# Performance work log

Measured on AMD Instinct MI355X. Metric: run time of the kernel, lower is better.

## Reference

```python
import jax, jax.numpy as jnp
import numpy as np

N = 50000      # nodes
E = 1_600_000  # edges
D = 512        # input_dim == embedding_dim (see notes: fc_emb output is dead code)
H = 256        # hidden_channels
G = 16         # graphs in the batch


def setup_inputs() -> dict:
    key = jax.random.key(0)
    ks = jax.random.split(key, 16)
    x = jax.random.normal(ks[0], (N, D), dtype=jnp.float32)
    edge_index = jax.random.randint(ks[1], (2, E), 0, N, dtype=jnp.int64)
    batch = jnp.sort(jax.random.randint(ks[2], (N,), 0, G, dtype=jnp.int64))

    def lin(k, fi, fo):
        s = 1.0 / np.sqrt(fi)
        return jax.random.uniform(k, (fi, fo), jnp.float32, -s, s)

    return {
        "x": x,
        "edge_index": edge_index,
        "batch": batch,
        "W1": lin(ks[3], D, H), "b1": jnp.zeros((H,), jnp.float32),
        "W2": lin(ks[4], H, H), "b2": jnp.zeros((H,), jnp.float32),
        "W3": lin(ks[5], H, H), "b3": jnp.zeros((H,), jnp.float32),
        "Wf": lin(ks[6], H, 64), "bf": jnp.zeros((64,), jnp.float32),
        "Wp": lin(ks[7], 64, 1), "bp": jnp.zeros((1,), jnp.float32),
    }


def _gcn_conv(h, src, dst, norm, W, b):
    # GCNConv: out[i] = sum_{j->i} norm_ji * (h[j] @ W) + b  (self-loops included in src/dst)
    m = h @ W                                    # [N, out]  transform first (smaller gather)
    agg = jax.ops.segment_sum(m[src] * norm[:, None], dst, num_segments=N)
    return agg + b


def reference(x, edge_index, batch, W1, b1, W2, b2, W3, b3, Wf, bf, Wp, bp):
    loops = jnp.arange(N, dtype=edge_index.dtype)
    src = jnp.concatenate([edge_index[0], loops])   # [E+N]
    dst = jnp.concatenate([edge_index[1], loops])
    # symmetric normalization D^{-1/2} (A+I) D^{-1/2}; degree over targets incl. self-loops
    deg = jax.ops.segment_sum(jnp.ones_like(dst, jnp.float32), dst, num_segments=N)
    dinv = jnp.where(deg > 0, jax.lax.rsqrt(deg), 0.0)
    norm = dinv[src] * dinv[dst]                    # [E+N]

    h = jax.nn.relu(_gcn_conv(x, src, dst, norm, W1, b1))
    h = jax.nn.relu(_gcn_conv(h, src, dst, norm, W2, b2))
    h = _gcn_conv(h, src, dst, norm, W3, b3)

    # global_mean_pool over graph ids
    counts = jax.ops.segment_sum(jnp.ones((N,), jnp.float32), batch, num_segments=G)
    pooled = jax.ops.segment_sum(h, batch, num_segments=G) / jnp.maximum(counts, 1.0)[:, None]

    # dropout treated as identity (eval-mode determinism for baseline)
    out = pooled @ Wf + bf
    out = out @ Wp + bp
    return jax.nn.sigmoid(out)
```

## Files before the change

kernel.cpp:

```cpp
#include <hip/hip_runtime.h>
#include <hip/hip_bf16.h>

#define NN 50000
#define EE 1600000
#define DD 512
#define HH 256
#define GG 16
#define BK 96
#define NCH 256
#define CHSZ 6250

typedef long fp8x8;
typedef __attribute__((ext_vector_type(4))) float f32x4;
typedef __attribute__((ext_vector_type(2))) float f32x2;

__device__ __forceinline__ float b2f(unsigned short s) {
    union { unsigned int i; float f; } v; v.i = ((unsigned int)s) << 16; return v.f;
}
__device__ __forceinline__ unsigned char f2fp8(float f) {
    return (unsigned char)(__builtin_amdgcn_cvt_pk_fp8_f32(f, f, 0, false) & 0xff);
}
__device__ __forceinline__ unsigned int pk4fp8(float a, float b, float c, float d) {
    unsigned int r = __builtin_amdgcn_cvt_pk_fp8_f32(a, b, 0, false);
    return __builtin_amdgcn_cvt_pk_fp8_f32(c, d, r, true);
}

__global__ __launch_bounds__(256) void k_hist_cvt(const int* __restrict__ ei,
                                                  unsigned int* __restrict__ histg,
                                                  const float* __restrict__ x, unsigned char* __restrict__ xb,
                                                  const float* __restrict__ W1, const float* __restrict__ W2,
                                                  const float* __restrict__ W3, unsigned char* __restrict__ W1t,
                                                  unsigned char* __restrict__ W2t, unsigned char* __restrict__ W3t) {
    __shared__ unsigned int hp[6250];
    int b = blockIdx.x, t = threadIdx.x;
    if (b < 1024) {
        int j = b >> 2, q = b & 3;
        int dlo = q * 12500;
        for (int i = t; i < 6250; i += 256) hp[i] = 0;
        __syncthreads();
        int base = j * CHSZ;
        for (int k = 0; k < 25; ++k) {
            int o = k * 256 + t;
            if (o < CHSZ) {
                int d = ei[EE + base + o];
                unsigned int ld = (unsigned)(d - dlo);
                if (ld < 12500u) atomicAdd(&hp[ld >> 1], (ld & 1) ? 65536u : 1u);
            }
        }
        __syncthreads();
        unsigned int* dst = histg + j * 25000 + q * 6250;
        for (int i = t; i < 6250; i += 256) dst[i] = hp[i];
    } else if (b < 7274) {
        size_t i0 = ((size_t)(b - 1024) * 256 + t) * 16;
        float4 v0 = *(const float4*)(x + i0);
        float4 v1 = *(const float4*)(x + i0 + 4);
        float4 v2 = *(const float4*)(x + i0 + 8);
        float4 v3 = *(const float4*)(x + i0 + 12);
        uint4 o;
        o.x = pk4fp8(v0.x, v0.y, v0.z, v0.w);
        o.y = pk4fp8(v1.x, v1.y, v1.z, v1.w);
        o.z = pk4fp8(v2.x, v2.y, v2.z, v2.w);
        o.w = pk4fp8(v3.x, v3.y, v3.z, v3.w);
        *(uint4*)(xb + i0) = o;
    } else {
        int u = (b - 7274) * 256 + t;
        if (u < 131072) {
            int k = u >> 8, n = u & 255;
            W1t[(size_t)n * 512 + k] = f2fp8(W1[u]);
        } else if (u < 196608) {
            int q = u - 131072; int k = q >> 8, n = q & 255;
            W2t[(size_t)n * 256 + k] = f2fp8(W2[q]);
        } else {
            int q = u - 196608; int k = q >> 8, n = q & 255;
            W3t[(size_t)n * 256 + k] = f2fp8(W3[q]);
        }
    }
}

__global__ __launch_bounds__(256) void k_scan(const unsigned int* __restrict__ histg,
                                              unsigned int* __restrict__ offg,
                                              int* __restrict__ cnt, float* __restrict__ dinv) {
    __shared__ unsigned int part[8][32];
    int t = threadIdx.x;
    int il = t & 31, g = t >> 5;
    int i = blockIdx.x * 32 + il;
    bool ok = (i < 25000);
    unsigned int hv[32];
    unsigned int p0 = 0, p1 = 0;
    if (ok) {
        const unsigned int* hp = histg + (size_t)(g * 32) * 25000 + i;
        #pragma unroll
        for (int jj = 0; jj < 32; ++jj) hv[jj] = hp[(size_t)jj * 25000];
        #pragma unroll
        for (int jj = 0; jj < 32; ++jj) { p0 += hv[jj] & 0xffffu; p1 += hv[jj] >> 16; }
    }
    part[g][il] = p0 | (p1 << 16);
    __syncthreads();
    unsigned int b0 = 0, b1 = 0;
    #pragma unroll
    for (int g2 = 0; g2 < 7; ++g2) {
        if (g2 < g) { unsigned int p = part[g2][il]; b0 += p & 0xffffu; b1 += p >> 16; }
    }
    if (ok && g == 7) {
        unsigned int tot0 = b0 + p0, tot1 = b1 + p1;
        cnt[2 * i]     = (int)tot0;
        cnt[2 * i + 1] = (int)tot1;
        dinv[2 * i]     = rsqrtf((float)tot0 + 1.0f);
        dinv[2 * i + 1] = rsqrtf((float)tot1 + 1.0f);
    }
    if (ok) {
        unsigned int run0 = b0, run1 = b1;
        unsigned int* op = offg + (size_t)(g * 32) * 25000 + i;
        #pragma unroll
        for (int jj = 0; jj < 32; ++jj) {
            op[(size_t)jj * 25000] = run0 | (run1 << 16);
            run0 += hv[jj] & 0xffffu; run1 += hv[jj] >> 16;
        }
    }
}

__global__ __launch_bounds__(256) void k_place(const int* __restrict__ ei,
                                               const unsigned int* __restrict__ offg,
                                               unsigned short* __restrict__ bucket) {
    __shared__ unsigned int cur[3125];
    int b = blockIdx.x, t = threadIdx.x;
    int x8 = b & 7, j = b >> 3;
    int lo = x8 * CHSZ;
    for (int i = t; i < 3125; i += 256) cur[i] = 0;
    __syncthreads();
    int base = j * CHSZ;
    for (int k = 0; k < 25; ++k) {
        int o = k * 256 + t;
        if (o < CHSZ) {
            int d = ei[EE + base + o];
            unsigned ld = (unsigned)(d - lo);
            if (ld < 6250u) {
                int s = ei[base + o];
                unsigned old = atomicAdd(&cur[ld >> 1], (ld & 1) ? 65536u : 1u);
                unsigned rank = (ld & 1) ? (old >> 16) : (old & 0xffffu);
                unsigned ov = offg[j * 25000 + (d >> 1)];
                unsigned pos = ((d & 1) ? (ov >> 16) : (ov & 0xffffu)) + rank;
                if (pos < BK) bucket[(size_t)d * BK + pos] = (unsigned short)s;
            }
        }
    }
}

__global__ __launch_bounds__(256) void k_gemm_fp8(const unsigned char* __restrict__ A,
                                                  const unsigned char* __restrict__ Bt,
                                                  const float* __restrict__ dinv,
                                                  unsigned char* __restrict__ C, int M, int K) {
    __shared__ unsigned char As[128 * 32];
    __shared__ unsigned char Bs[128 * 32];
    const int tid  = threadIdx.x;
    const int wave = tid >> 6;
    const int lane = tid & 63;
    const int row0 = blockIdx.x * 128;
    const int col0 = blockIdx.y * 128;
    const int wr = wave & 1;
    const int wc = wave >> 1;
    const int l15 = lane & 15;
    const int quad = lane >> 4;

    const int sr = tid >> 1;
    const int sk = (tid & 1) * 16;

    int ar = row0 + sr; if (ar >= M) ar = M - 1;
    const int bc = col0 + sr;

    f32x4 acc[4][4];
    #pragma unroll
    for (int i = 0; i < 4; ++i)
        #pragma unroll
        for (int j = 0; j < 4; ++j)
            acc[i][j] = (f32x4){0.f, 0.f, 0.f, 0.f};

    for (int kb = 0; kb < K; kb += 32) {
        const unsigned char* ga = A + (size_t)ar * K + kb + sk;
        const unsigned char* gb = Bt + (size_t)bc * K + kb + sk;
        __builtin_amdgcn_global_load_lds((const __attribute__((address_space(1))) void*)ga,
            (__attribute__((address_space(3))) void*)&As[wave * 1024], 16, 0, 0);
        __builtin_amdgcn_global_load_lds((const __attribute__((address_space(1))) void*)gb,
            (__attribute__((address_space(3))) void*)&Bs[wave * 1024], 16, 0, 0);
        __syncthreads();

        fp8x8 af[4], bfr[4];
        #pragma unroll
        for (int mi = 0; mi < 4; ++mi)
            af[mi] = *(const fp8x8*)&As[(wr * 64 + mi * 16 + l15) * 32 + quad * 8];
        #pragma unroll
        for (int ni = 0; ni < 4; ++ni)
            bfr[ni] = *(const fp8x8*)&Bs[(wc * 64 + ni * 16 + l15) * 32 + quad * 8];
        #pragma unroll
        for (int mi = 0; mi < 4; ++mi)
            #pragma unroll
            for (int ni = 0; ni < 4; ++ni)
                acc[mi][ni] = __builtin_amdgcn_mfma_f32_16x16x32_fp8_fp8(af[mi], bfr[ni], acc[mi][ni], 0, 0, 0);
        __syncthreads();
    }

    #pragma unroll
    for (int mi = 0; mi < 4; ++mi) {
        #pragma unroll
        for (int r = 0; r < 4; ++r) {
            int grow = row0 + wr * 64 + mi * 16 + quad * 4 + r;
            if (grow < M) {
                float ds = dinv[grow];
                #pragma unroll
                for (int ni = 0; ni < 4; ++ni) {
                    int gcol = col0 + wc * 64 + ni * 16 + l15;
                    C[(size_t)grow * 256 + gcol] = f2fp8(ds * acc[mi][ni][r]);
                }
            }
        }
    }
}

__global__ __launch_bounds__(256) void k_agg(const unsigned int* __restrict__ m,
                                             const float* __restrict__ bias,
                                             const float* __restrict__ dinv, const int* __restrict__ cnt,
                                             const unsigned short* __restrict__ bucket,
                                             unsigned int* __restrict__ outb,
                                             int do_relu) {
    int lane = threadIdx.x & 63;
    int node = blockIdx.x * 4 + (threadIdx.x >> 6);
    if (node >= NN) return;
    const unsigned int* mrow = m + lane;
    unsigned int v = mrow[(size_t)node * 64];
    f32x2 lo = __builtin_amdgcn_cvt_pk_f32_fp8(v, false);
    f32x2 hi = __builtin_amdgcn_cvt_pk_f32_fp8(v, true);
    float4 acc = make_float4(lo.x, lo.y, hi.x, hi.y);
    int n = cnt[node]; if (n > BK) n = BK;
    const unsigned short* cs = bucket + (size_t)node * BK;
    int p = 0;
    for (; p + 8 <= n; p += 8) {
        int s0 = cs[p], s1 = cs[p + 1], s2 = cs[p + 2], s3 = cs[p + 3];
        int s4 = cs[p + 4], s5 = cs[p + 5], s6 = cs[p + 6], s7 = cs[p + 7];
        unsigned int u0 = mrow[(size_t)s0 * 64];
        unsigned int u1 = mrow[(size_t)s1 * 64];
        unsigned int u2 = mrow[(size_t)s2 * 64];
        unsigned int u3 = mrow[(size_t)s3 * 64];
        unsigned int u4 = mrow[(size_t)s4 * 64];
        unsigned int u5 = mrow[(size_t)s5 * 64];
        unsigned int u6 = mrow[(size_t)s6 * 64];
        unsigned int u7 = mrow[(size_t)s7 * 64];
        f32x2 a0 = __builtin_amdgcn_cvt_pk_f32_fp8(u0, false), b0 = __builtin_amdgcn_cvt_pk_f32_fp8(u0, true);
        f32x2 a1 = __builtin_amdgcn_cvt_pk_f32_fp8(u1, false), b1 = __builtin_amdgcn_cvt_pk_f32_fp8(u1, true);
        f32x2 a2 = __builtin_amdgcn_cvt_pk_f32_fp8(u2, false), b2 = __builtin_amdgcn_cvt_pk_f32_fp8(u2, true);
        f32x2 a3 = __builtin_amdgcn_cvt_pk_f32_fp8(u3, false), b3 = __builtin_amdgcn_cvt_pk_f32_fp8(u3, true);
        f32x2 a4 = __builtin_amdgcn_cvt_pk_f32_fp8(u4, false), b4 = __builtin_amdgcn_cvt_pk_f32_fp8(u4, true);
        f32x2 a5 = __builtin_amdgcn_cvt_pk_f32_fp8(u5, false), b5 = __builtin_amdgcn_cvt_pk_f32_fp8(u5, true);
        f32x2 a6 = __builtin_amdgcn_cvt_pk_f32_fp8(u6, false), b6 = __builtin_amdgcn_cvt_pk_f32_fp8(u6, true);
        f32x2 a7 = __builtin_amdgcn_cvt_pk_f32_fp8(u7, false), b7 = __builtin_amdgcn_cvt_pk_f32_fp8(u7, true);
        acc.x += ((a0.x + a1.x) + (a2.x + a3.x)) + ((a4.x + a5.x) + (a6.x + a7.x));
        acc.y += ((a0.y + a1.y) + (a2.y + a3.y)) + ((a4.y + a5.y) + (a6.y + a7.y));
        acc.z += ((b0.x + b1.x) + (b2.x + b3.x)) + ((b4.x + b5.x) + (b6.x + b7.x));
        acc.w += ((b0.y + b1.y) + (b2.y + b3.y)) + ((b4.y + b5.y) + (b6.y + b7.y));
    }
    for (; p < n; ++p) {
        int s = cs[p];
        unsigned int u = mrow[(size_t)s * 64];
        f32x2 a = __builtin_amdgcn_cvt_pk_f32_fp8(u, false);
        f32x2 b = __builtin_amdgcn_cvt_pk_f32_fp8(u, true);
        acc.x += a.x; acc.y += a.y; acc.z += b.x; acc.w += b.y;
    }
    float di = dinv[node];
    const float4 bb = *(const float4*)(bias + lane * 4);
    acc.x = acc.x * di + bb.x; acc.y = acc.y * di + bb.y;
    acc.z = acc.z * di + bb.z; acc.w = acc.w * di + bb.w;
    if (do_relu) {
        acc.x = fmaxf(acc.x, 0.f); acc.y = fmaxf(acc.y, 0.f);
        acc.z = fmaxf(acc.z, 0.f); acc.w = fmaxf(acc.w, 0.f);
    }
    outb[(size_t)node * 64 + lane] = pk4fp8(acc.x, acc.y, acc.z, acc.w);
}

__global__ __launch_bounds__(256) void k_pool(const unsigned int* __restrict__ h,
                                              const int* __restrict__ batch,
                                              float* __restrict__ pooled, float* __restrict__ cnts) {
    __shared__ float pl[GG * 256];
    __shared__ float cl[GG];
    int t = threadIdx.x;
    for (int i = t; i < GG * 256; i += 256) pl[i] = 0.f;
    if (t < GG) cl[t] = 0.f;
    __syncthreads();
    int sub = t >> 6;
    int fd = t & 63;
    int chunk = (NN + gridDim.x - 1) / gridDim.x;
    int i0 = blockIdx.x * chunk;
    int i1 = i0 + chunk; if (i1 > NN) i1 = NN;
    int gcur = -1;
    float a0 = 0.f, a1 = 0.f, a2 = 0.f, a3 = 0.f, cr = 0.f;
    for (int i = i0 + sub; i < i1; i += 4) {
        int g = batch[i];
        if (g != gcur) {
            if (gcur >= 0) {
                atomicAdd(&pl[gcur * 256 + fd * 4 + 0], a0);
                atomicAdd(&pl[gcur * 256 + fd * 4 + 1], a1);
                atomicAdd(&pl[gcur * 256 + fd * 4 + 2], a2);
                atomicAdd(&pl[gcur * 256 + fd * 4 + 3], a3);
                if (fd == 0) atomicAdd(&cl[gcur], cr);
            }
            gcur = g; a0 = a1 = a2 = a3 = 0.f; cr = 0.f;
        }
        unsigned int u = h[(size_t)i * 64 + fd];
        f32x2 lo = __builtin_amdgcn_cvt_pk_f32_fp8(u, false);
        f32x2 hi = __builtin_amdgcn_cvt_pk_f32_fp8(u, true);
        a0 += lo.x; a1 += lo.y; a2 += hi.x; a3 += hi.y;
        cr += 1.f;
    }
    if (gcur >= 0) {
        atomicAdd(&pl[gcur * 256 + fd * 4 + 0], a0);
        atomicAdd(&pl[gcur * 256 + fd * 4 + 1], a1);
        atomicAdd(&pl[gcur * 256 + fd * 4 + 2], a2);
        atomicAdd(&pl[gcur * 256 + fd * 4 + 3], a3);
        if (fd == 0) atomicAdd(&cl[gcur], cr);
    }
    __syncthreads();
    for (int i = t; i < GG * 256; i += 256)
        if (pl[i] != 0.f) atomicAdd(&pooled[i], pl[i]);
    if (t < GG && cl[t] != 0.f) atomicAdd(&cnts[t], cl[t]);
}

__global__ __launch_bounds__(1024) void k_head(const float* __restrict__ pooled, const float* __restrict__ cnts,
                                               const float* __restrict__ Wf, const float* __restrict__ bf,
                                               const float* __restrict__ Wp, const float* __restrict__ bp,
                                               float* __restrict__ out) {
    __shared__ float z[GG][64];
    int t = threadIdx.x;
    int g = t >> 6, j = t & 63;
    float inv = 1.f / fmaxf(cnts[g], 1.f);
    float acc = 0.f;
    for (int k = 0; k < 256; ++k) acc += pooled[g * 256 + k] * Wf[k * 64 + j];
    z[g][j] = acc * inv + bf[j];
    __syncthreads();
    if (t < GG) {
        float o = 0.f;
        for (int j2 = 0; j2 < 64; ++j2) o += z[t][j2] * Wp[j2];
        o += bp[0];
        out[t] = 1.f / (1.f + expf(-o));
    }
}

extern "C" void kernel_launch(void* const* d_in, const int* in_sizes, int n_in,
                              void* d_out, int out_size, void* d_ws, size_t ws_size,
                              hipStream_t stream) {
    const float* x   = (const float*)d_in[0];
    const int*   ei  = (const int*)d_in[1];
    const int*   bat = (const int*)d_in[2];
    const float* W1  = (const float*)d_in[3];
    const float* b1  = (const float*)d_in[4];
    const float* W2  = (const float*)d_in[5];
    const float* b2  = (const float*)d_in[6];
    const float* W3  = (const float*)d_in[7];
    const float* b3  = (const float*)d_in[8];
    const float* Wf  = (const float*)d_in[9];
    const float* bf  = (const float*)d_in[10];
    const float* Wp  = (const float*)d_in[11];
    const float* bp  = (const float*)d_in[12];
    float* out = (float*)d_out;

    char* w = (char*)d_ws;
    unsigned char* xb  = (unsigned char*)w;  w += (size_t)NN * DD;
    unsigned char* mb  = (unsigned char*)w;  w += (size_t)NN * HH;
    unsigned char* hb  = (unsigned char*)w;  w += (size_t)NCH * 25000 * 4;
    unsigned char* hb2 = (unsigned char*)w;  w += (size_t)NCH * 25000 * 4;
    unsigned char* W1t = (unsigned char*)w;  w += (size_t)DD * HH;
    unsigned char* W2t = (unsigned char*)w;  w += (size_t)HH * HH;
    unsigned char* W3t = (unsigned char*)w;  w += (size_t)HH * HH;
    float* dinv   = (float*)w;               w += (size_t)NN * 4;
    int*   cnt    = (int*)w;                 w += (size_t)NN * 4;
    unsigned short* bucket = (unsigned short*)w; w += (size_t)NN * BK * 2;
    float* pooled = (float*)w;               w += (size_t)GG * HH * 4;
    float* cnts   = (float*)w;               w += (size_t)GG * 4;

    unsigned int* histg = (unsigned int*)hb;
    unsigned int* offg  = (unsigned int*)hb2;

    hipMemsetAsync(pooled, 0, (size_t)(GG * HH + GG) * 4, stream);

    k_hist_cvt<<<8298, 256, 0, stream>>>(ei, histg, x, xb, W1, W2, W3, W1t, W2t, W3t);
    k_scan<<<782, 256, 0, stream>>>(histg, offg, cnt, dinv);
    k_place<<<2048, 256, 0, stream>>>(ei, offg, bucket);

    dim3 gg((NN + 127) / 128, 2);
    k_gemm_fp8<<<gg, 256, 0, stream>>>(xb, W1t, dinv, mb, NN, DD);
    k_agg<<<(NN + 3) / 4, 256, 0, stream>>>((const unsigned int*)mb, b1, dinv, cnt, bucket,
                                            (unsigned int*)hb, 1);
    k_gemm_fp8<<<gg, 256, 0, stream>>>(hb, W2t, dinv, mb, NN, HH);
    k_agg<<<(NN + 3) / 4, 256, 0, stream>>>((const unsigned int*)mb, b2, dinv, cnt, bucket,
                                            (unsigned int*)hb2, 1);
    k_gemm_fp8<<<gg, 256, 0, stream>>>(hb2, W3t, dinv, mb, NN, HH);
    k_agg<<<(NN + 3) / 4, 256, 0, stream>>>((const unsigned int*)mb, b3, dinv, cnt, bucket,
                                            (unsigned int*)hb, 0);

    k_pool<<<256, 256, 0, stream>>>((const unsigned int*)hb, bat, pooled, cnts);
    k_head<<<1, 1024, 0, stream>>>(pooled, cnts, Wf, bf, Wp, bp, out);
}
```

Measured before the change: 546.2 us.

## Fuse histogram, scan, and placement into one cooperative kernel with grid syncs

Replaces the three CSR-building kernels with a single cooperative kernel that uses grid-wide syncs between the histogram, scan and placement phases. Per-chunk histograms are now packed four 8-bit counters per word, so each block covers the full node range instead of splitting by quarters or eighths, and each edge chunk is read by one block rather than four or eight. The x and weight FP8 conversion is handed out through an atomic ticket to fill idle time after the histogram phase. The aim is to cut launch overhead and redundant edge reads. In exchange it risks overflow of the 8-bit counters when one chunk has more than 255 edges to a single node, and it relies on all 768 blocks being co-resident for the cooperative launch.

Measured after the change: 808.9 us. +48.1%, slower.

```diff
diff --git a/kernel.cpp b/kernel.cpp
--- a/kernel.cpp
+++ b/kernel.cpp
@@ -1,5 +1,8 @@
 #include <hip/hip_runtime.h>
 #include <hip/hip_bf16.h>
+#include <hip/hip_cooperative_groups.h>
+
+namespace cg = cooperative_groups;
 
 #define NN 50000
 #define EE 1600000
@@ -10,13 +13,15 @@
 #define NCH 256
 #define CHSZ 6250
 
+#define NBLD 768
+#define NUNIT_X 6250
+#define NUNIT_W 64
+#define NUNITS (NUNIT_X + NUNIT_W)
+
 typedef long fp8x8;
 typedef __attribute__((ext_vector_type(4))) float f32x4;
 typedef __attribute__((ext_vector_type(2))) float f32x2;
 
-__device__ __forceinline__ float b2f(unsigned short s) {
-    union { unsigned int i; float f; } v; v.i = ((unsigned int)s) << 16; return v.f;
-}
 __device__ __forceinline__ unsigned char f2fp8(float f) {
     return (unsigned char)(__builtin_amdgcn_cvt_pk_fp8_f32(f, f, 0, false) & 0xff);
 }
@@ -25,120 +30,126 @@
     return __builtin_amdgcn_cvt_pk_fp8_f32(c, d, r, true);
 }
 
-__global__ __launch_bounds__(256) void k_hist_cvt(const int* __restrict__ ei,
-                                                  unsigned int* __restrict__ histg,
-                                                  const float* __restrict__ x, unsigned char* __restrict__ xb,
-                                                  const float* __restrict__ W1, const float* __restrict__ W2,
-                                                  const float* __restrict__ W3, unsigned char* __restrict__ W1t,
-                                                  unsigned char* __restrict__ W2t, unsigned char* __restrict__ W3t) {
-    __shared__ unsigned int hp[6250];
-    int b = blockIdx.x, t = threadIdx.x;
-    if (b < 1024) {
-        int j = b >> 2, q = b & 3;
-        int dlo = q * 12500;
-        for (int i = t; i < 6250; i += 256) hp[i] = 0;
-        __syncthreads();
-        int base = j * CHSZ;
+__global__ __launch_bounds__(256) void k_build(const int* __restrict__ ei,
+    unsigned int* __restrict__ histg,
+    unsigned int* __restrict__ offg,
+    int* __restrict__ cnt, float* __restrict__ dinv,
+    unsigned short* __restrict__ bucket,
+    const float* __restrict__ x, unsigned char* __restrict__ xb,
+    const float* __restrict__ W1, const float* __restrict__ W2, const float* __restrict__ W3,
+    unsigned char* __restrict__ W1t, unsigned char* __restrict__ W2t, unsigned char* __restrict__ W3t,
+    unsigned int* __restrict__ gticket)
+{
+    __shared__ unsigned int sh[12500];
+    const int b = blockIdx.x, t = threadIdx.x;
+
+    if (b < NCH) {
+        for (int i = t; i < 12500; i += 256) sh[i] = 0u;
+        __syncthreads();
+        const int base = b * CHSZ;
         for (int k = 0; k < 25; ++k) {
             int o = k * 256 + t;
             if (o < CHSZ) {
                 int d = ei[EE + base + o];
-                unsigned int ld = (unsigned)(d - dlo);
-                if (ld < 12500u) atomicAdd(&hp[ld >> 1], (ld & 1) ? 65536u : 1u);
-            }
-        }
-        __syncthreads();
-        unsigned int* dst = histg + j * 25000 + q * 6250;
-        for (int i = t; i < 6250; i += 256) dst[i] = hp[i];
-    } else if (b < 7274) {
-        size_t i0 = ((size_t)(b - 1024) * 256 + t) * 16;
-        float4 v0 = *(const float4*)(x + i0);
-        float4 v1 = *(const float4*)(x + i0 + 4);
-        float4 v2 = *(const float4*)(x + i0 + 8);
-        float4 v3 = *(const float4*)(x + i0 + 12);
-        uint4 o;
-        o.x = pk4fp8(v0.x, v0.y, v0.z, v0.w);
-        o.y = pk4fp8(v1.x, v1.y, v1.z, v1.w);
-        o.z = pk4fp8(v2.x, v2.y, v2.z, v2.w);
-        o.w = pk4fp8(v3.x, v3.y, v3.z, v3.w);
-        *(uint4*)(xb + i0) = o;
-    } else {
-        int u = (b - 7274) * 256 + t;
-        if (u < 131072) {
-            int k = u >> 8, n = u & 255;
-            W1t[(size_t)n * 512 + k] = f2fp8(W1[u]);
-        } else if (u < 196608) {
-            int q = u - 131072; int k = q >> 8, n = q & 255;
-            W2t[(size_t)n * 256 + k] = f2fp8(W2[q]);
+                atomicAdd(&sh[d >> 2], 1u << ((d & 3) * 8));
+            }
+        }
+        __syncthreads();
+        unsigned int* hrow = histg + (size_t)b * 12500;
+        for (int i = t; i < 12500; i += 256) hrow[i] = sh[i];
+    }
+    for (;;) {
+        __syncthreads();
+        if (t == 0) sh[0] = atomicAdd(gticket, 1u);
+        __syncthreads();
+        unsigned int u = sh[0];
+        if (u >= NUNITS) break;
+        if (u < NUNIT_X) {
+            size_t i0 = ((size_t)u * 256 + t) * 16;
+            float4 v0 = *(const float4*)(x + i0);
+            float4 v1 = *(const float4*)(x + i0 + 4);
+            float4 v2 = *(const float4*)(x + i0 + 8);
+            float4 v3 = *(const float4*)(x + i0 + 12);
+            uint4 o;
+            o.x = pk4fp8(v0.x, v0.y, v0.z, v0.w);
+            o.y = pk4fp8(v1.x, v1.y, v1.z, v1.w);
+            o.z = pk4fp8(v2.x, v2.y, v2.z, v2.w);
+            o.w = pk4fp8(v3.x, v3.y, v3.z, v3.w);
+            *(uint4*)(xb + i0) = o;
         } else {
-            int q = u - 196608; int k = q >> 8, n = q & 255;
-            W3t[(size_t)n * 256 + k] = f2fp8(W3[q]);
-        }
-    }
-}
-
-__global__ __launch_bounds__(256) void k_scan(const unsigned int* __restrict__ histg,
-                                              unsigned int* __restrict__ offg,
-                                              int* __restrict__ cnt, float* __restrict__ dinv) {
-    __shared__ unsigned int part[8][32];
-    int t = threadIdx.x;
-    int il = t & 31, g = t >> 5;
-    int i = blockIdx.x * 32 + il;
-    bool ok = (i < 25000);
-    unsigned int hv[32];
-    unsigned int p0 = 0, p1 = 0;
-    if (ok) {
-        const unsigned int* hp = histg + (size_t)(g * 32) * 25000 + i;
-        #pragma unroll
-        for (int jj = 0; jj < 32; ++jj) hv[jj] = hp[(size_t)jj * 25000];
-        #pragma unroll
-        for (int jj = 0; jj < 32; ++jj) { p0 += hv[jj] & 0xffffu; p1 += hv[jj] >> 16; }
-    }
-    part[g][il] = p0 | (p1 << 16);
-    __syncthreads();
-    unsigned int b0 = 0, b1 = 0;
-    #pragma unroll
-    for (int g2 = 0; g2 < 7; ++g2) {
-        if (g2 < g) { unsigned int p = part[g2][il]; b0 += p & 0xffffu; b1 += p >> 16; }
-    }
-    if (ok && g == 7) {
-        unsigned int tot0 = b0 + p0, tot1 = b1 + p1;
-        cnt[2 * i]     = (int)tot0;
-        cnt[2 * i + 1] = (int)tot1;
-        dinv[2 * i]     = rsqrtf((float)tot0 + 1.0f);
-        dinv[2 * i + 1] = rsqrtf((float)tot1 + 1.0f);
-    }
-    if (ok) {
-        unsigned int run0 = b0, run1 = b1;
-        unsigned int* op = offg + (size_t)(g * 32) * 25000 + i;
-        #pragma unroll
-        for (int jj = 0; jj < 32; ++jj) {
-            op[(size_t)jj * 25000] = run0 | (run1 << 16);
-            run0 += hv[jj] & 0xffffu; run1 += hv[jj] >> 16;
-        }
-    }
-}
-
-__global__ __launch_bounds__(256) void k_place(const int* __restrict__ ei,
-                                               const unsigned int* __restrict__ offg,
-                                               unsigned short* __restrict__ bucket) {
-    __shared__ unsigned int cur[3125];
-    int b = blockIdx.x, t = threadIdx.x;
-    int x8 = b & 7, j = b >> 3;
-    int lo = x8 * CHSZ;
-    for (int i = t; i < 3125; i += 256) cur[i] = 0;
-    __syncthreads();
-    int base = j * CHSZ;
-    for (int k = 0; k < 25; ++k) {
-        int o = k * 256 + t;
-        if (o < CHSZ) {
-            int d = ei[EE + base + o];
-            unsigned ld = (unsigned)(d - lo);
-            if (ld < 6250u) {
+            int wu = u - NUNIT_X;
+            #pragma unroll
+            for (int c = 0; c < 16; ++c) {
+                int e = wu * 4096 + c * 256 + t;
+                if (e < 131072) {
+                    int k = e >> 8, n = e & 255;
+                    W1t[(size_t)n * 512 + k] = f2fp8(W1[e]);
+                } else if (e < 196608) {
+                    int q = e - 131072; int k = q >> 8, n = q & 255;
+                    W2t[(size_t)n * 256 + k] = f2fp8(W2[q]);
+                } else {
+                    int q = e - 196608; int k = q >> 8, n = q & 255;
+                    W3t[(size_t)n * 256 + k] = f2fp8(W3[q]);
+                }
+            }
+        }
+    }
+    cg::this_grid().sync();
+
+    if (b < 391) {
+        const int il = t & 31, g = t >> 5;
+        const int g4 = b * 32 + il;
+        const bool ok = (g4 < 12500);
+        unsigned hv[32];
+        unsigned s02 = 0, s13 = 0;
+        if (ok) {
+            const unsigned* hp = histg + (size_t)(g * 32) * 12500 + g4;
+            #pragma unroll
+            for (int jj = 0; jj < 32; ++jj) hv[jj] = hp[(size_t)jj * 12500];
+            #pragma unroll
+            for (int jj = 0; jj < 32; ++jj) { s02 += hv[jj] & 0x00ff00ffu; s13 += (hv[jj] >> 8) & 0x00ff00ffu; }
+        }
+        sh[t * 2] = s02; sh[t * 2 + 1] = s13;
+        __syncthreads();
+        unsigned b02 = 0, b13 = 0;
+        #pragma unroll
+        for (int g2 = 0; g2 < 7; ++g2)
+            if (g2 < g) { b02 += sh[(g2 * 32 + il) * 2]; b13 += sh[(g2 * 32 + il) * 2 + 1]; }
+        if (ok && g == 7) {
+            unsigned t02 = b02 + s02, t13 = b13 + s13;
+            int4 cv; cv.x = (int)(t02 & 0xffffu); cv.y = (int)(t13 & 0xffffu);
+            cv.z = (int)(t02 >> 16);      cv.w = (int)(t13 >> 16);
+            *(int4*)(cnt + 4 * g4) = cv;
+            float4 dv;
+            dv.x = rsqrtf((float)cv.x + 1.0f); dv.y = rsqrtf((float)cv.y + 1.0f);
+            dv.z = rsqrtf((float)cv.z + 1.0f); dv.w = rsqrtf((float)cv.w + 1.0f);
+            *(float4*)(dinv + 4 * g4) = dv;
+        }
+        if (ok) {
+            unsigned r0 = b02 & 0xffffu, r2 = b02 >> 16, r1 = b13 & 0xffffu, r3 = b13 >> 16;
+            #pragma unroll
+            for (int jj = 0; jj < 32; ++jj) {
+                uint2 wv; wv.x = r0 | (r1 << 16); wv.y = r2 | (r3 << 16);
+                *(uint2*)(offg + (size_t)(g * 32 + jj) * 25000 + 2 * g4) = wv;
+                unsigned h = hv[jj];
+                r0 += h & 0xffu; r1 += (h >> 8) & 0xffu; r2 += (h >> 16) & 0xffu; r3 += h >> 24;
+            }
+        }
+    }
+    cg::this_grid().sync();
+
+    if (b < NCH) {
+        for (int i = t; i < 12500; i += 256) sh[i] = 0u;
+        __syncthreads();
+        const int base = b * CHSZ;
+        for (int k = 0; k < 25; ++k) {
+            int o = k * 256 + t;
+            if (o < CHSZ) {
+                int d = ei[EE + base + o];
                 int s = ei[base + o];
-                unsigned old = atomicAdd(&cur[ld >> 1], (ld & 1) ? 65536u : 1u);
-                unsigned rank = (ld & 1) ? (old >> 16) : (old & 0xffffu);
-                unsigned ov = offg[j * 25000 + (d >> 1)];
+                unsigned old = atomicAdd(&sh[d >> 2], 1u << ((d & 3) * 8));
+                unsigned rank = (old >> ((d & 3) * 8)) & 0xffu;
+                unsigned ov = offg[(size_t)b * 25000 + (d >> 1)];
                 unsigned pos = ((d & 1) ? (ov >> 16) : (ov & 0xffffu)) + rank;
                 if (pos < BK) bucket[(size_t)d * BK + pos] = (unsigned short)s;
             }
@@ -373,15 +384,20 @@
     unsigned short* bucket = (unsigned short*)w; w += (size_t)NN * BK * 2;
     float* pooled = (float*)w;               w += (size_t)GG * HH * 4;
     float* cnts   = (float*)w;               w += (size_t)GG * 4;
+    unsigned int* gticket = (unsigned int*)w; w += 4;
 
     unsigned int* histg = (unsigned int*)hb;
     unsigned int* offg  = (unsigned int*)hb2;
 
-    hipMemsetAsync(pooled, 0, (size_t)(GG * HH + GG) * 4, stream);
-
-    k_hist_cvt<<<8298, 256, 0, stream>>>(ei, histg, x, xb, W1, W2, W3, W1t, W2t, W3t);
-    k_scan<<<782, 256, 0, stream>>>(histg, offg, cnt, dinv);
-    k_place<<<2048, 256, 0, stream>>>(ei, offg, bucket);
+    hipMemsetAsync(pooled, 0, (size_t)(GG * HH + GG + 1) * 4, stream);
+
+    {
+        void* args[] = { (void*)&ei, (void*)&histg, (void*)&offg, (void*)&cnt, (void*)&dinv,
+                         (void*)&bucket, (void*)&x, (void*)&xb,
+                         (void*)&W1, (void*)&W2, (void*)&W3,
+                         (void*)&W1t, (void*)&W2t, (void*)&W3t, (void*)&gticket };
+        hipLaunchCooperativeKernel((void*)k_build, dim3(NBLD), dim3(256), args, 0, stream);
+    }
 
     dim3 gg((NN + 127) / 128, 2);
     k_gemm_fp8<<<gg, 256, 0, stream>>>(xb, W1t, dinv, mb, NN, DD);
```

## Double-buffer FP8 GEMM with swizzled LDS tiles and widen aggregation index loads

Applied to the files above, without the earlier changes.

The FP8 GEMM now stages 64-wide K tiles into double-buffered LDS with an XOR swizzle, prefetching the next tile while MFMAs run on the current one. This halves the barrier count and is meant to hide global load latency. The aggregation kernel loads neighbor indices as 16-byte vectors and adds a 16-way unrolled gather loop to raise memory-level parallelism. The trade-offs are more LDS per block and more registers, which may reduce occupancy, and the vector index loads rely on the bucket rows being 16-byte aligned.

After: 518.5 us. -5.1%, faster.

```diff
diff --git a/kernel.cpp b/kernel.cpp
--- a/kernel.cpp
+++ b/kernel.cpp
@@ -14,9 +14,6 @@
 typedef __attribute__((ext_vector_type(4))) float f32x4;
 typedef __attribute__((ext_vector_type(2))) float f32x2;
 
-__device__ __forceinline__ float b2f(unsigned short s) {
-    union { unsigned int i; float f; } v; v.i = ((unsigned int)s) << 16; return v.f;
-}
 __device__ __forceinline__ unsigned char f2fp8(float f) {
     return (unsigned char)(__builtin_amdgcn_cvt_pk_fp8_f32(f, f, 0, false) & 0xff);
 }
@@ -150,8 +147,8 @@
                                                   const unsigned char* __restrict__ Bt,
                                                   const float* __restrict__ dinv,
                                                   unsigned char* __restrict__ C, int M, int K) {
-    __shared__ unsigned char As[128 * 32];
-    __shared__ unsigned char Bs[128 * 32];
+    __shared__ unsigned char As[2][8192];
+    __shared__ unsigned char Bs[2][8192];
     const int tid  = threadIdx.x;
     const int wave = tid >> 6;
     const int lane = tid & 63;
@@ -162,11 +159,27 @@
     const int l15 = lane & 15;
     const int quad = lane >> 4;
 
-    const int sr = tid >> 1;
-    const int sk = (tid & 1) * 16;
-
-    int ar = row0 + sr; if (ar >= M) ar = M - 1;
-    const int bc = col0 + sr;
+    const int srow = (wave << 4) + (lane >> 2);
+    const int gk16 = (((lane & 3) ^ (srow & 3)) << 4);
+    int arow1 = row0 + srow;      if (arow1 >= M) arow1 = M - 1;
+    int arow2 = row0 + srow + 64; if (arow2 >= M) arow2 = M - 1;
+    const int brow1 = col0 + srow;
+    const int brow2 = brow1 + 64;
+
+#define STAGE(BUF, KB) do {                                                              \
+    const unsigned char* ga1_ = A  + (size_t)arow1 * K + (KB) + gk16;                    \
+    const unsigned char* ga2_ = A  + (size_t)arow2 * K + (KB) + gk16;                    \
+    const unsigned char* gb1_ = Bt + (size_t)brow1 * K + (KB) + gk16;                    \
+    const unsigned char* gb2_ = Bt + (size_t)brow2 * K + (KB) + gk16;                    \
+    __builtin_amdgcn_global_load_lds((const __attribute__((address_space(1))) void*)ga1_,\
+        (__attribute__((address_space(3))) void*)&As[BUF][wave * 1024], 16, 0, 0);       \
+    __builtin_amdgcn_global_load_lds((const __attribute__((address_space(1))) void*)ga2_,\
+        (__attribute__((address_space(3))) void*)&As[BUF][4096 + wave * 1024], 16, 0, 0);\
+    __builtin_amdgcn_global_load_lds((const __attribute__((address_space(1))) void*)gb1_,\
+        (__attribute__((address_space(3))) void*)&Bs[BUF][wave * 1024], 16, 0, 0);       \
+    __builtin_amdgcn_global_load_lds((const __attribute__((address_space(1))) void*)gb2_,\
+        (__attribute__((address_space(3))) void*)&Bs[BUF][4096 + wave * 1024], 16, 0, 0);\
+} while (0)
 
     f32x4 acc[4][4];
     #pragma unroll
@@ -175,29 +188,35 @@
         for (int j = 0; j < 4; ++j)
             acc[i][j] = (f32x4){0.f, 0.f, 0.f, 0.f};
 
-    for (int kb = 0; kb < K; kb += 32) {
-        const unsigned char* ga = A + (size_t)ar * K + kb + sk;
-        const unsigned char* gb = Bt + (size_t)bc * K + kb + sk;
-        __builtin_amdgcn_global_load_lds((const __attribute__((address_space(1))) void*)ga,
-            (__attribute__((address_space(3))) void*)&As[wave * 1024], 16, 0, 0);
-        __builtin_amdgcn_global_load_lds((const __attribute__((address_space(1))) void*)gb,
-            (__attribute__((address_space(3))) void*)&Bs[wave * 1024], 16, 0, 0);
+    const int NT = K >> 6;
+    STAGE(0, 0);
+    __syncthreads();
+
+    for (int t = 0; t < NT; ++t) {
+        const int cb = t & 1;
+        if (t + 1 < NT) STAGE(cb ^ 1, (t + 1) << 6);
+
+        fp8x8 af[2][4], bfr[2][4];
+        #pragma unroll
+        for (int kk = 0; kk < 2; ++kk) {
+            const int csw = (((kk * 2 + (quad >> 1)) ^ (l15 & 3)) << 4) + ((quad & 1) << 3);
+            #pragma unroll
+            for (int mi = 0; mi < 4; ++mi) {
+                af[kk][mi]  = *(const fp8x8*)&As[cb][(wr * 64 + mi * 16 + l15) * 64 + csw];
+                bfr[kk][mi] = *(const fp8x8*)&Bs[cb][(wc * 64 + mi * 16 + l15) * 64 + csw];
+            }
+        }
+        #pragma unroll
+        for (int kk = 0; kk < 2; ++kk)
+            #pragma unroll
+            for (int mi = 0; mi < 4; ++mi)
+                #pragma unroll
+                for (int ni = 0; ni < 4; ++ni)
+                    acc[mi][ni] = __builtin_amdgcn_mfma_f32_16x16x32_fp8_fp8(af[kk][mi], bfr[kk][ni], acc[mi][ni], 0, 0, 0);
+
         __syncthreads();
-
-        fp8x8 af[4], bfr[4];
-        #pragma unroll
-        for (int mi = 0; mi < 4; ++mi)
-            af[mi] = *(const fp8x8*)&As[(wr * 64 + mi * 16 + l15) * 32 + quad * 8];
-        #pragma unroll
-        for (int ni = 0; ni < 4; ++ni)
-            bfr[ni] = *(const fp8x8*)&Bs[(wc * 64 + ni * 16 + l15) * 32 + quad * 8];
-        #pragma unroll
-        for (int mi = 0; mi < 4; ++mi)
-            #pragma unroll
-            for (int ni = 0; ni < 4; ++ni)
-                acc[mi][ni] = __builtin_amdgcn_mfma_f32_16x16x32_fp8_fp8(af[mi], bfr[ni], acc[mi][ni], 0, 0, 0);
-        __syncthreads();
-    }
+    }
+#undef STAGE
 
     #pragma unroll
     for (int mi = 0; mi < 4; ++mi) {
@@ -233,17 +252,60 @@
     int n = cnt[node]; if (n > BK) n = BK;
     const unsigned short* cs = bucket + (size_t)node * BK;
     int p = 0;
+    for (; p + 16 <= n; p += 16) {
+        uint4 iv0 = *(const uint4*)(cs + p);
+        uint4 iv1 = *(const uint4*)(cs + p + 8);
+        unsigned int u0 = mrow[(size_t)(iv0.x & 0xffffu) * 64];
+        unsigned int u1 = mrow[(size_t)(iv0.x >> 16)    * 64];
+        unsigned int u2 = mrow[(size_t)(iv0.y & 0xffffu) * 64];
+        unsigned int u3 = mrow[(size_t)(iv0.y >> 16)    * 64];
+        unsigned int u4 = mrow[(size_t)(iv0.z & 0xffffu) * 64];
+        unsigned int u5 = mrow[(size_t)(iv0.z >> 16)    * 64];
+        unsigned int u6 = mrow[(size_t)(iv0.w & 0xffffu) * 64];
+        unsigned int u7 = mrow[(size_t)(iv0.w >> 16)    * 64];
+        unsigned int u8 = mrow[(size_t)(iv1.x & 0xffffu) * 64];
+        unsigned int u9 = mrow[(size_t)(iv1.x >> 16)    * 64];
+        unsigned int ua = mrow[(size_t)(iv1.y & 0xffffu) * 64];
+        unsigned int ub = mrow[(size_t)(iv1.y >> 16)    * 64];
+        unsigned int uc = mrow[(size_t)(iv1.z & 0xffffu) * 64];
+        unsigned int ud = mrow[(size_t)(iv1.z >> 16)    * 64];
+        unsigned int ue = mrow[(size_t)(iv1.w & 0xffffu) * 64];
+        unsigned int uf = mrow[(size_t)(iv1.w >> 16)    * 64];
+        f32x2 a0 = __builtin_amdgcn_cvt_pk_f32_fp8(u0, false), b0 = __builtin_amdgcn_cvt_pk_f32_fp8(u0, true);
+        f32x2 a1 = __builtin_amdgcn_cvt_pk_f32_fp8(u1, false), b1 = __builtin_amdgcn_cvt_pk_f32_fp8(u1, true);
+        f32x2 a2 = __builtin_amdgcn_cvt_pk_f32_fp8(u2, false), b2 = __builtin_amdgcn_cvt_pk_f32_fp8(u2, true);
+        f32x2 a3 = __builtin_amdgcn_cvt_pk_f32_fp8(u3, false), b3 = __builtin_amdgcn_cvt_pk_f32_fp8(u3, true);
+        f32x2 a4 = __builtin_amdgcn_cvt_pk_f32_fp8(u4, false), b4 = __builtin_amdgcn_cvt_pk_f32_fp8(u4, true);
+        f32x2 a5 = __builtin_amdgcn_cvt_pk_f32_fp8(u5, false), b5 = __builtin_amdgcn_cvt_pk_f32_fp8(u5, true);
+        f32x2 a6 = __builtin_amdgcn_cvt_pk_f32_fp8(u6, false), b6 = __builtin_amdgcn_cvt_pk_f32_fp8(u6, true);
+        f32x2 a7 = __builtin_amdgcn_cvt_pk_f32_fp8(u7, false), b7 = __builtin_amdgcn_cvt_pk_f32_fp8(u7, true);
+        f32x2 a8 = __builtin_amdgcn_cvt_pk_f32_fp8(u8, false), b8 = __builtin_amdgcn_cvt_pk_f32_fp8(u8, true);
+        f32x2 a9 = __builtin_amdgcn_cvt_pk_f32_fp8(u9, false), b9 = __builtin_amdgcn_cvt_pk_f32_fp8(u9, true);
+        f32x2 aa = __builtin_amdgcn_cvt_pk_f32_fp8(ua, false), ba = __builtin_amdgcn_cvt_pk_f32_fp8(ua, true);
+        f32x2 ab = __builtin_amdgcn_cvt_pk_f32_fp8(ub, false), bb2 = __builtin_amdgcn_cvt_pk_f32_fp8(ub, true);
+        f32x2 ac = __builtin_amdgcn_cvt_pk_f32_fp8(uc, false), bc = __builtin_amdgcn_cvt_pk_f32_fp8(uc, true);
+        f32x2 ad = __builtin_amdgcn_cvt_pk_f32_fp8(ud, false), bd = __builtin_amdgcn_cvt_pk_f32_fp8(ud, true);
+        f32x2 ae = __builtin_amdgcn_cvt_pk_f32_fp8(ue, false), be = __builtin_amdgcn_cvt_pk_f32_fp8(ue, true);
+        f32x2 af2 = __builtin_amdgcn_cvt_pk_f32_fp8(uf, false), bf2 = __builtin_amdgcn_cvt_pk_f32_fp8(uf, true);
+        acc.x += (((a0.x + a1.x) + (a2.x + a3.x)) + ((a4.x + a5.x) + (a6.x + a7.x)))
+               + (((a8.x + a9.x) + (aa.x + ab.x)) + ((ac.x + ad.x) + (ae.x + af2.x)));
+        acc.y += (((a0.y + a1.y) + (a2.y + a3.y)) + ((a4.y + a5.y) + (a6.y + a7.y)))
+               + (((a8.y + a9.y) + (aa.y + ab.y)) + ((ac.y + ad.y) + (ae.y + af2.y)));
+        acc.z += (((b0.x + b1.x) + (b2.x + b3.x)) + ((b4.x + b5.x) + (b6.x + b7.x)))
+               + (((b8.x + b9.x) + (ba.x + bb2.x)) + ((bc.x + bd.x) + (be.x + bf2.x)));
+        acc.w += (((b0.y + b1.y) + (b2.y + b3.y)) + ((b4.y + b5.y) + (b6.y + b7.y)))
+               + (((b8.y + b9.y) + (ba.y + bb2.y)) + ((bc.y + bd.y) + (be.y + bf2.y)));
+    }
     for (; p + 8 <= n; p += 8) {
-        int s0 = cs[p], s1 = cs[p + 1], s2 = cs[p + 2], s3 = cs[p + 3];
-        int s4 = cs[p + 4], s5 = cs[p + 5], s6 = cs[p + 6], s7 = cs[p + 7];
-        unsigned int u0 = mrow[(size_t)s0 * 64];
-        unsigned int u1 = mrow[(size_t)s1 * 64];
-        unsigned int u2 = mrow[(size_t)s2 * 64];
-        unsigned int u3 = mrow[(size_t)s3 * 64];
-        unsigned int u4 = mrow[(size_t)s4 * 64];
-        unsigned int u5 = mrow[(size_t)s5 * 64];
-        unsigned int u6 = mrow[(size_t)s6 * 64];
-        unsigned int u7 = mrow[(size_t)s7 * 64];
+        uint4 iv0 = *(const uint4*)(cs + p);
+        unsigned int u0 = mrow[(size_t)(iv0.x & 0xffffu) * 64];
+        unsigned int u1 = mrow[(size_t)(iv0.x >> 16)    * 64];
+        unsigned int u2 = mrow[(size_t)(iv0.y & 0xffffu) * 64];
+        unsigned int u3 = mrow[(size_t)(iv0.y >> 16)    * 64];
+        unsigned int u4 = mrow[(size_t)(iv0.z & 0xffffu) * 64];
+        unsigned int u5 = mrow[(size_t)(iv0.z >> 16)    * 64];
+        unsigned int u6 = mrow[(size_t)(iv0.w & 0xffffu) * 64];
+        unsigned int u7 = mrow[(size_t)(iv0.w >> 16)    * 64];
         f32x2 a0 = __builtin_amdgcn_cvt_pk_f32_fp8(u0, false), b0 = __builtin_amdgcn_cvt_pk_f32_fp8(u0, true);
         f32x2 a1 = __builtin_amdgcn_cvt_pk_f32_fp8(u1, false), b1 = __builtin_amdgcn_cvt_pk_f32_fp8(u1, true);
         f32x2 a2 = __builtin_amdgcn_cvt_pk_f32_fp8(u2, false), b2 = __builtin_amdgcn_cvt_pk_f32_fp8(u2, true);
```
